# Kernel optimization log

Measured on AMD Instinct MI355X. Metric: run time of the kernel, lower is better.

The kernel has to match this reference:

```python
import jax, jax.numpy as jnp
import numpy as np

B, H, W, DIM = 8, 1024, 1024, 33


def setup_inputs() -> dict:
    key = jax.random.key(0)
    x = jax.random.uniform(key, (B, 3, H, W), dtype=jnp.float32)
    # Identity 3D LUT matching IdentityLUT{dim}.txt layout: n = i*D*D + j*D + k,
    # channel0 = k/(D-1) (red), channel1 = j/(D-1) (green), channel2 = i/(D-1) (blue).
    ax = jnp.arange(DIM, dtype=jnp.float32) / (DIM - 1)
    i, j, k = jnp.meshgrid(ax, ax, ax, indexing='ij')
    LUT = jnp.stack([k, j, i], axis=0)  # [3, D, D, D]
    return {"x": x, "LUT": LUT}


def _trilinear_lut(LUT, x):
    # LUT: [3, D, D, D] with spatial axes (i=depth, j=height, k=width).
    # x:   [B, 3, H, W] in [0,1]. grid_sample grid coord order is (w, h, d),
    # so red -> k axis, green -> j axis, blue -> i axis.
    D = LUT.shape[1]
    g = (x - 0.5) * 2.0                       # [-1, 1] grid (as in torch code)
    t = (g + 1.0) * 0.5 * (D - 1)             # align_corners=True unnormalize
    t = jnp.clip(t, 0.0, D - 1)               # padding_mode='border'
    r, gc, b = t[:, 0], t[:, 1], t[:, 2]      # each [B, H, W]

    def floor_ceil(c):
        f = jnp.floor(c)
        w = c - f
        f = f.astype(jnp.int32)
        return f, jnp.minimum(f + 1, D - 1), w

    k0, k1, wk = floor_ceil(r)
    j0, j1, wj = floor_ceil(gc)
    i0, i1, wi = floor_ceil(b)

    flat = LUT.reshape(3, -1)                 # [3, D^3]

    def gather(ii, jj, kk):
        idx = (ii * D + jj) * D + kk          # [B, H, W]
        return flat[:, idx]                   # [3, B, H, W]

    c00 = gather(i0, j0, k0) * (1 - wk) + gather(i0, j0, k1) * wk
    c01 = gather(i0, j1, k0) * (1 - wk) + gather(i0, j1, k1) * wk
    c10 = gather(i1, j0, k0) * (1 - wk) + gather(i1, j0, k1) * wk
    c11 = gather(i1, j1, k0) * (1 - wk) + gather(i1, j1, k1) * wk
    out = (c00 * (1 - wj) + c01 * wj) * (1 - wi) + (c10 * (1 - wj) + c11 * wj) * wi
    return jnp.transpose(out, (1, 0, 2, 3))   # [B, 3, H, W]


def reference(x, LUT):
    return _trilinear_lut(LUT, x)
```

## Files before the change

### kernel.cpp

```cpp
#include <hip/hip_runtime.h>
#include <hip/hip_fp16.h>

constexpr int D      = 33;
constexpr int LUTSZ  = D * D * D;
constexpr int PLANE  = 1024 * 1024;
constexpr int BATCH  = 8;
constexpr int NCELL  = 32 * 32 * 32;
constexpr size_t CELL_BYTES   = (size_t)NCELL * 32;
constexpr size_t PACKED_BYTES = (size_t)LUTSZ * 16;

constexpr int NITER = 4;

typedef float        v4f  __attribute__((ext_vector_type(4)));
typedef unsigned int v4u  __attribute__((ext_vector_type(4)));
typedef unsigned int v2u  __attribute__((ext_vector_type(2)));
typedef int          i32x4 __attribute__((ext_vector_type(4)));

__device__ v4u llvm_amdgcn_raw_buffer_load_u32x4(i32x4 srsrc, int voffset,
                                                 int soffset, int cachepolicy)
    __asm("llvm.amdgcn.raw.buffer.load.v4i32");

struct Rgb   { float c0, c1, c2; };
struct CellW { int cell; float wk, wj, wi; };

__device__ __forceinline__ unsigned int pack_h2(float lo, float hi)
{
    __half2 h = __floats2half2_rn(lo, hi);
    return *reinterpret_cast<unsigned int*>(&h);
}

__device__ __forceinline__ float h_lo(unsigned int u)
{
    __half2 h = *reinterpret_cast<__half2*>(&u);
    return __half2float(__low2half(h));
}

__device__ __forceinline__ float h_hi(unsigned int u)
{
    __half2 h = *reinterpret_cast<__half2*>(&u);
    return __half2float(__high2half(h));
}

__global__ __launch_bounds__(256)
void pack_cells_kernel(const float* __restrict__ lut, unsigned char* __restrict__ Tb)
{
    const int cell = blockIdx.x * blockDim.x + threadIdx.x;
    const int ch   = blockIdx.y;
    if (cell >= NCELL) return;
    const int i0 = cell >> 10, j0 = (cell >> 5) & 31, k0 = cell & 31;
    const int base = (i0 * D + j0) * D + k0;

    const float* __restrict__ L = lut + ch * LUTSZ + base;
    const float anchor = L[0];
    const float d1 = L[1]             - anchor;
    const float d2 = L[D]             - anchor;
    const float d3 = L[D + 1]         - anchor;
    const float d4 = L[D * D]         - anchor;
    const float d5 = L[D * D + 1]     - anchor;
    const float d6 = L[D * D + D]     - anchor;
    const float d7 = L[D * D + D + 1] - anchor;

    unsigned int wa = (unsigned int)__builtin_amdgcn_cvt_pk_fp8_f32(d1, d2, 0, false);
    wa = (unsigned int)__builtin_amdgcn_cvt_pk_fp8_f32(d3, d4, (int)wa, true);
    unsigned int wb = (unsigned int)__builtin_amdgcn_cvt_pk_fp8_f32(d5, d6, 0, false);
    wb = (unsigned int)__builtin_amdgcn_cvt_pk_fp8_f32(d7, 0.0f, (int)wb, true);

    unsigned char* __restrict__ e = Tb + (size_t)cell * 32;
    *reinterpret_cast<__half*>(e + 2 * ch) = __float2half(anchor);
    v2u dw; dw.x = wa; dw.y = wb;
    *reinterpret_cast<v2u*>(e + 8 + 8 * ch) = dw;
}

__device__ __forceinline__ CellW cell_of(float r, float g, float b)
{
    float tr = fminf(fmaxf(r * 32.0f, 0.0f), 32.0f);
    float tg = fminf(fmaxf(g * 32.0f, 0.0f), 32.0f);
    float tb = fminf(fmaxf(b * 32.0f, 0.0f), 32.0f);

    int k0 = min((int)tr, 31);
    int j0 = min((int)tg, 31);
    int i0 = min((int)tb, 31);
    CellW w;
    w.wk = tr - (float)k0;
    w.wj = tg - (float)j0;
    w.wi = tb - (float)i0;
    w.cell = ((i0 << 5) | j0) << 5 | k0;
    return w;
}

template <int SEL>
__device__ __forceinline__ float f8c(unsigned int w)
{
    return __builtin_amdgcn_cvt_f32_fp8((int)w, SEL);
}

__device__ __forceinline__ float chan_lerp(float a, unsigned int wa, unsigned int wb,
                                           float wk, float wj, float wi)
{
    const float d001 = f8c<0>(wa), d010 = f8c<1>(wa), d011 = f8c<2>(wa), d100 = f8c<3>(wa);
    const float d101 = f8c<0>(wb), d110 = f8c<1>(wb), d111 = f8c<2>(wb);
    const float L00 = wk * d001;
    const float L01 = fmaf(wk, d011 - d010, d010);
    const float L10 = fmaf(wk, d101 - d100, d100);
    const float L11 = fmaf(wk, d111 - d110, d110);
    const float c0  = fmaf(wj, L01 - L00, L00);
    const float c1  = fmaf(wj, L11 - L10, L10);
    return a + fmaf(wi, c1 - c0, c0);
}

__device__ __forceinline__ Rgb lerp_cell(v4u ea, v4u eb, CellW w)
{
    Rgb o;
    const float a0 = h_lo(ea.x), a1 = h_hi(ea.x), a2 = h_lo(ea.y);
    o.c0 = chan_lerp(a0, ea.z, ea.w, w.wk, w.wj, w.wi);
    o.c1 = chan_lerp(a1, eb.x, eb.y, w.wk, w.wj, w.wi);
    o.c2 = chan_lerp(a2, eb.z, eb.w, w.wk, w.wj, w.wi);
    return o;
}

__global__ __launch_bounds__(256)
void lut3d_cell_kernel(const float* __restrict__ x,
                       const v4u* __restrict__ T,
                       float* __restrict__ out)
{
    const int tid    = blockIdx.x * blockDim.x + threadIdx.x;
    const int stride = gridDim.x * blockDim.x;

    const unsigned long long ta = (unsigned long long)T;
    i32x4 rsrc;
    rsrc.x = (int)(ta & 0xffffffffull);
    rsrc.y = (int)(ta >> 32);
    rsrc.z = (int)CELL_BYTES;
    rsrc.w = 0x00020000;

    int c = tid;
    int base;
    v4f rv, gv, bv;
    {
        const int p0 = c << 2;
        const int b  = p0 >> 20;
        const int q  = p0 & (PLANE - 1);
        base = b * 3 * PLANE + q;
        rv = __builtin_nontemporal_load(reinterpret_cast<const v4f*>(x + base));
        gv = __builtin_nontemporal_load(reinterpret_cast<const v4f*>(x + base + PLANE));
        bv = __builtin_nontemporal_load(reinterpret_cast<const v4f*>(x + base + 2 * PLANE));
    }

#pragma unroll
    for (int it = 0; it < NITER; ++it) {
        const CellW w0 = cell_of(rv.x, gv.x, bv.x);
        const CellW w1 = cell_of(rv.y, gv.y, bv.y);
        const CellW w2 = cell_of(rv.z, gv.z, bv.z);
        const CellW w3 = cell_of(rv.w, gv.w, bv.w);

        const int o0v = w0.cell << 5, o1v = w1.cell << 5;
        const int o2v = w2.cell << 5, o3v = w3.cell << 5;
        const v4u e0a = llvm_amdgcn_raw_buffer_load_u32x4(rsrc, o0v,      0, 1);
        const v4u e0b = llvm_amdgcn_raw_buffer_load_u32x4(rsrc, o0v + 16, 0, 1);
        const v4u e1a = llvm_amdgcn_raw_buffer_load_u32x4(rsrc, o1v,      0, 1);
        const v4u e1b = llvm_amdgcn_raw_buffer_load_u32x4(rsrc, o1v + 16, 0, 1);
        const v4u e2a = llvm_amdgcn_raw_buffer_load_u32x4(rsrc, o2v,      0, 1);
        const v4u e2b = llvm_amdgcn_raw_buffer_load_u32x4(rsrc, o2v + 16, 0, 1);
        const v4u e3a = llvm_amdgcn_raw_buffer_load_u32x4(rsrc, o3v,      0, 1);
        const v4u e3b = llvm_amdgcn_raw_buffer_load_u32x4(rsrc, o3v + 16, 0, 1);

        const int cn = c + stride;
        int basen = base;
        v4f rn = rv, gn = gv, bn = bv;
        if (it + 1 < NITER) {
            const int p0 = cn << 2;
            const int b  = p0 >> 20;
            const int q  = p0 & (PLANE - 1);
            basen = b * 3 * PLANE + q;
            rn = __builtin_nontemporal_load(reinterpret_cast<const v4f*>(x + basen));
            gn = __builtin_nontemporal_load(reinterpret_cast<const v4f*>(x + basen + PLANE));
            bn = __builtin_nontemporal_load(reinterpret_cast<const v4f*>(x + basen + 2 * PLANE));
        }
        __builtin_amdgcn_sched_barrier(0);

        const Rgb q0 = lerp_cell(e0a, e0b, w0);
        const Rgb q1 = lerp_cell(e1a, e1b, w1);
        const Rgb q2 = lerp_cell(e2a, e2b, w2);
        const Rgb q3 = lerp_cell(e3a, e3b, w3);

        v4f o0 = { q0.c0, q1.c0, q2.c0, q3.c0 };
        v4f o1 = { q0.c1, q1.c1, q2.c1, q3.c1 };
        v4f o2 = { q0.c2, q1.c2, q2.c2, q3.c2 };
        __builtin_nontemporal_store(o0, reinterpret_cast<v4f*>(out + base));
        __builtin_nontemporal_store(o1, reinterpret_cast<v4f*>(out + base + PLANE));
        __builtin_nontemporal_store(o2, reinterpret_cast<v4f*>(out + base + 2 * PLANE));

        rv = rn; gv = gn; bv = bn; base = basen; c = cn;
    }
}

__global__ __launch_bounds__(256)
void pack_lut_kernel(const float* __restrict__ lut, v4u* __restrict__ P)
{
    int idx = blockIdx.x * blockDim.x + threadIdx.x;
    if (idx >= LUTSZ) return;
    int k = idx % D;
    v4u e = (v4u)(0u);
    if (k < D - 1) {
        e.x = pack_h2(lut[0 * LUTSZ + idx], lut[0 * LUTSZ + idx + 1]);
        e.y = pack_h2(lut[1 * LUTSZ + idx], lut[1 * LUTSZ + idx + 1]);
        e.z = pack_h2(lut[2 * LUTSZ + idx], lut[2 * LUTSZ + idx + 1]);
    }
    P[idx] = e;
}

__device__ __forceinline__ float lerp_h2(unsigned int u, float w)
{
    __half2 h = *reinterpret_cast<__half2*>(&u);
    float lo = __half2float(__low2half(h));
    float hi = __half2float(__high2half(h));
    return fmaf(w, hi - lo, lo);
}

__device__ __forceinline__ Rgb apply_lut_packed(const v4u* __restrict__ P,
                                                float r, float g, float b)
{
    float tr = fminf(fmaxf(r * 32.0f, 0.0f), 32.0f);
    float tg = fminf(fmaxf(g * 32.0f, 0.0f), 32.0f);
    float tb = fminf(fmaxf(b * 32.0f, 0.0f), 32.0f);
    int k0 = min((int)tr, D - 2); float wk = tr - (float)k0;
    int j0 = (int)tg; float wj = tg - (float)j0; int j1 = min(j0 + 1, D - 1);
    int i0 = (int)tb; float wi = tb - (float)i0; int i1 = min(i0 + 1, D - 1);
    v4u e00 = P[(i0 * D + j0) * D + k0];
    v4u e01 = P[(i0 * D + j1) * D + k0];
    v4u e10 = P[(i1 * D + j0) * D + k0];
    v4u e11 = P[(i1 * D + j1) * D + k0];
    Rgb o;
    {
        float c00 = lerp_h2(e00.x, wk), c01 = lerp_h2(e01.x, wk);
        float c10 = lerp_h2(e10.x, wk), c11 = lerp_h2(e11.x, wk);
        float c0 = fmaf(wj, c01 - c00, c00), c1 = fmaf(wj, c11 - c10, c10);
        o.c0 = fmaf(wi, c1 - c0, c0);
    }
    {
        float c00 = lerp_h2(e00.y, wk), c01 = lerp_h2(e01.y, wk);
        float c10 = lerp_h2(e10.y, wk), c11 = lerp_h2(e11.y, wk);
        float c0 = fmaf(wj, c01 - c00, c00), c1 = fmaf(wj, c11 - c10, c10);
        o.c1 = fmaf(wi, c1 - c0, c0);
    }
    {
        float c00 = lerp_h2(e00.z, wk), c01 = lerp_h2(e01.z, wk);
        float c10 = lerp_h2(e10.z, wk), c11 = lerp_h2(e11.z, wk);
        float c0 = fmaf(wj, c01 - c00, c00), c1 = fmaf(wj, c11 - c10, c10);
        o.c2 = fmaf(wi, c1 - c0, c0);
    }
    return o;
}

__global__ __launch_bounds__(256)
void lut3d_packed_kernel(const float* __restrict__ x,
                         const v4u* __restrict__ P,
                         float* __restrict__ out)
{
    const int tid = blockIdx.x * blockDim.x + threadIdx.x;
    const int p0  = tid << 2;
    const int b   = p0 >> 20;
    const int q   = p0 & (PLANE - 1);
    const int base = b * 3 * PLANE + q;
    const v4f rv = __builtin_nontemporal_load(reinterpret_cast<const v4f*>(x + base));
    const v4f gv = __builtin_nontemporal_load(reinterpret_cast<const v4f*>(x + base + PLANE));
    const v4f bv = __builtin_nontemporal_load(reinterpret_cast<const v4f*>(x + base + 2 * PLANE));
    Rgb p0r = apply_lut_packed(P, rv.x, gv.x, bv.x);
    Rgb p1r = apply_lut_packed(P, rv.y, gv.y, bv.y);
    Rgb p2r = apply_lut_packed(P, rv.z, gv.z, bv.z);
    Rgb p3r = apply_lut_packed(P, rv.w, gv.w, bv.w);
    v4f o0 = { p0r.c0, p1r.c0, p2r.c0, p3r.c0 };
    v4f o1 = { p0r.c1, p1r.c1, p2r.c1, p3r.c1 };
    v4f o2 = { p0r.c2, p1r.c2, p2r.c2, p3r.c2 };
    __builtin_nontemporal_store(o0, reinterpret_cast<v4f*>(out + base));
    __builtin_nontemporal_store(o1, reinterpret_cast<v4f*>(out + base + PLANE));
    __builtin_nontemporal_store(o2, reinterpret_cast<v4f*>(out + base + 2 * PLANE));
}

extern "C" void kernel_launch(void* const* d_in, const int* in_sizes, int n_in,
                              void* d_out, int out_size, void* d_ws, size_t ws_size,
                              hipStream_t stream)
{
    const float* x   = (const float*)d_in[0];
    const float* lut = (const float*)d_in[1];
    float* out       = (float*)d_out;

    if (ws_size >= CELL_BYTES) {
        pack_cells_kernel<<<dim3(NCELL / 256, 3), 256, 0, stream>>>(
            lut, (unsigned char*)d_ws);
        const int n_chunks  = (BATCH * PLANE) / 4;
        const int n_threads = n_chunks / NITER;
        lut3d_cell_kernel<<<n_threads / 256, 256, 0, stream>>>(x, (const v4u*)d_ws, out);
    } else if (ws_size >= PACKED_BYTES) {
        v4u* P = (v4u*)d_ws;
        pack_lut_kernel<<<(LUTSZ + 255) / 256, 256, 0, stream>>>(lut, P);
        const int n_threads = (BATCH * PLANE) / 4;
        lut3d_packed_kernel<<<n_threads / 256, 256, 0, stream>>>(x, P, out);
    }
}
```

Before: 214.9 us.

## Split LUT cells into linear part and skippable cross-term corrections

Re-expresses each cell's trilinear interpolation as an anchor plus linear terms plus cross-term corrections (wj*wk, wi*wk, wi*wj, wi*wj*wk). The linear part for all three channels now packs into one 16-byte entry, so the main path issues one gather per pixel instead of two. Correction coefficients sit in a second table that is read only when a per-cell flag says they are nonzero for some lane in the wavefront. For the identity LUT the corrections are zero, so the second gather and its arithmetic are skipped. Arbitrary LUTs still take the exact path, at the cost of a divergent branch and an extra load.

Measured after the change: 211.1 us. About the same (-1.8%).

```diff
diff --git a/kernel.cpp b/kernel.cpp
--- a/kernel.cpp
+++ b/kernel.cpp
@@ -6,14 +6,15 @@
 constexpr int PLANE  = 1024 * 1024;
 constexpr int BATCH  = 8;
 constexpr int NCELL  = 32 * 32 * 32;
-constexpr size_t CELL_BYTES   = (size_t)NCELL * 32;
+constexpr size_t A_BYTES      = (size_t)NCELL * 16;
+constexpr size_t B_BYTES      = (size_t)NCELL * 16;
+constexpr size_t CELL_BYTES   = A_BYTES + B_BYTES;
 constexpr size_t PACKED_BYTES = (size_t)LUTSZ * 16;
 
 constexpr int NITER = 4;
 
 typedef float        v4f  __attribute__((ext_vector_type(4)));
 typedef unsigned int v4u  __attribute__((ext_vector_type(4)));
-typedef unsigned int v2u  __attribute__((ext_vector_type(2)));
 typedef int          i32x4 __attribute__((ext_vector_type(4)));
 
 __device__ v4u llvm_amdgcn_raw_buffer_load_u32x4(i32x4 srsrc, int voffset,
@@ -41,34 +42,86 @@
     return __half2float(__high2half(h));
 }
 
+template <int SEL>
+__device__ __forceinline__ float f8c(unsigned int w)
+{
+    return __builtin_amdgcn_cvt_f32_fp8((int)w, SEL);
+}
+
 __global__ __launch_bounds__(256)
-void pack_cells_kernel(const float* __restrict__ lut, unsigned char* __restrict__ Tb)
+void pack_cells_kernel(const float* __restrict__ lut,
+                       v4u* __restrict__ A, v4u* __restrict__ Bt)
 {
     const int cell = blockIdx.x * blockDim.x + threadIdx.x;
-    const int ch   = blockIdx.y;
     if (cell >= NCELL) return;
     const int i0 = cell >> 10, j0 = (cell >> 5) & 31, k0 = cell & 31;
     const int base = (i0 * D + j0) * D + k0;
 
-    const float* __restrict__ L = lut + ch * LUTSZ + base;
-    const float anchor = L[0];
-    const float d1 = L[1]             - anchor;
-    const float d2 = L[D]             - anchor;
-    const float d3 = L[D + 1]         - anchor;
-    const float d4 = L[D * D]         - anchor;
-    const float d5 = L[D * D + 1]     - anchor;
-    const float d6 = L[D * D + D]     - anchor;
-    const float d7 = L[D * D + D + 1] - anchor;
-
-    unsigned int wa = (unsigned int)__builtin_amdgcn_cvt_pk_fp8_f32(d1, d2, 0, false);
-    wa = (unsigned int)__builtin_amdgcn_cvt_pk_fp8_f32(d3, d4, (int)wa, true);
-    unsigned int wb = (unsigned int)__builtin_amdgcn_cvt_pk_fp8_f32(d5, d6, 0, false);
-    wb = (unsigned int)__builtin_amdgcn_cvt_pk_fp8_f32(d7, 0.0f, (int)wb, true);
-
-    unsigned char* __restrict__ e = Tb + (size_t)cell * 32;
-    *reinterpret_cast<__half*>(e + 2 * ch) = __float2half(anchor);
-    v2u dw; dw.x = wa; dw.y = wb;
-    *reinterpret_cast<v2u*>(e + 8 + 8 * ch) = dw;
+    float a[3], p001[3], p010[3], p100[3];
+    float c011[3], c101[3], c110[3], c111[3];
+    bool corr = false;
+#pragma unroll
+    for (int ch = 0; ch < 3; ++ch) {
+        const float* __restrict__ L = lut + ch * LUTSZ + base;
+        const float an   = L[0];
+        const float d001 = L[1]             - an;
+        const float d010 = L[D]             - an;
+        const float d011 = L[D + 1]         - an;
+        const float d100 = L[D * D]         - an;
+        const float d101 = L[D * D + 1]     - an;
+        const float d110 = L[D * D + D]     - an;
+        const float d111 = L[D * D + D + 1] - an;
+        a[ch] = an;  p001[ch] = d001;  p010[ch] = d010;  p100[ch] = d100;
+        c011[ch] = d011 - d010 - d001;
+        c101[ch] = d101 - d100 - d001;
+        c110[ch] = d110 - d100 - d010;
+        c111[ch] = d111 - d110 - d101 - d011 + d100 + d010 + d001;
+        corr = corr || (c011[ch] != 0.0f) || (c101[ch] != 0.0f)
+                    || (c110[ch] != 0.0f) || (c111[ch] != 0.0f);
+    }
+
+    v4u ea;
+    ea.x = pack_h2(a[0], a[1]);
+    {
+        unsigned int w = pack_h2(a[2], 0.0f) & 0xffffu;
+        w = (unsigned int)__builtin_amdgcn_cvt_pk_fp8_f32(p001[0], p010[0],
+                                                          (int)w, true);
+        ea.y = w;
+    }
+    {
+        unsigned int w = (unsigned int)__builtin_amdgcn_cvt_pk_fp8_f32(
+                             p100[0], p001[1], 0, false);
+        w = (unsigned int)__builtin_amdgcn_cvt_pk_fp8_f32(p010[1], p100[1],
+                                                          (int)w, true);
+        ea.z = w;
+    }
+    {
+        unsigned int w = (unsigned int)__builtin_amdgcn_cvt_pk_fp8_f32(
+                             p001[2], p010[2], 0, false);
+        w = (unsigned int)__builtin_amdgcn_cvt_pk_fp8_f32(p100[2], 0.0f,
+                                                          (int)w, true);
+        if (corr) w |= 0x01000000u;
+        ea.w = w;
+    }
+    A[cell] = ea;
+
+    v4u eb;
+    {
+        unsigned int w0 = (unsigned int)__builtin_amdgcn_cvt_pk_fp8_f32(
+                              c011[0], c101[0], 0, false);
+        w0 = (unsigned int)__builtin_amdgcn_cvt_pk_fp8_f32(c110[0], c111[0],
+                                                           (int)w0, true);
+        unsigned int w1 = (unsigned int)__builtin_amdgcn_cvt_pk_fp8_f32(
+                              c011[1], c101[1], 0, false);
+        w1 = (unsigned int)__builtin_amdgcn_cvt_pk_fp8_f32(c110[1], c111[1],
+                                                           (int)w1, true);
+        unsigned int w2 = (unsigned int)__builtin_amdgcn_cvt_pk_fp8_f32(
+                              c011[2], c101[2], 0, false);
+        w2 = (unsigned int)__builtin_amdgcn_cvt_pk_fp8_f32(c110[2], c111[2],
+                                                           (int)w2, true);
+        eb.x = w0; eb.y = w1; eb.z = w2; eb.w = 0u;
+    }
+    Bt[cell] = eb;
 }
 
 __device__ __forceinline__ CellW cell_of(float r, float g, float b)
@@ -88,49 +141,53 @@
     return w;
 }
 
-template <int SEL>
-__device__ __forceinline__ float f8c(unsigned int w)
-{
-    return __builtin_amdgcn_cvt_f32_fp8((int)w, SEL);
-}
-
-__device__ __forceinline__ float chan_lerp(float a, unsigned int wa, unsigned int wb,
-                                           float wk, float wj, float wi)
-{
-    const float d001 = f8c<0>(wa), d010 = f8c<1>(wa), d011 = f8c<2>(wa), d100 = f8c<3>(wa);
-    const float d101 = f8c<0>(wb), d110 = f8c<1>(wb), d111 = f8c<2>(wb);
-    const float L00 = wk * d001;
-    const float L01 = fmaf(wk, d011 - d010, d010);
-    const float L10 = fmaf(wk, d101 - d100, d100);
-    const float L11 = fmaf(wk, d111 - d110, d110);
-    const float c0  = fmaf(wj, L01 - L00, L00);
-    const float c1  = fmaf(wj, L11 - L10, L10);
-    return a + fmaf(wi, c1 - c0, c0);
-}
-
-__device__ __forceinline__ Rgb lerp_cell(v4u ea, v4u eb, CellW w)
+__device__ __forceinline__ Rgb lerp_planar(v4u ea, CellW w)
 {
     Rgb o;
     const float a0 = h_lo(ea.x), a1 = h_hi(ea.x), a2 = h_lo(ea.y);
-    o.c0 = chan_lerp(a0, ea.z, ea.w, w.wk, w.wj, w.wi);
-    o.c1 = chan_lerp(a1, eb.x, eb.y, w.wk, w.wj, w.wi);
-    o.c2 = chan_lerp(a2, eb.z, eb.w, w.wk, w.wj, w.wi);
+    {
+        const float s = fmaf(w.wj, f8c<3>(ea.y), w.wi * f8c<0>(ea.z));
+        o.c0 = a0 + fmaf(w.wk, f8c<2>(ea.y), s);
+    }
+    {
+        const float s = fmaf(w.wj, f8c<2>(ea.z), w.wi * f8c<3>(ea.z));
+        o.c1 = a1 + fmaf(w.wk, f8c<1>(ea.z), s);
+    }
+    {
+        const float s = fmaf(w.wj, f8c<1>(ea.w), w.wi * f8c<2>(ea.w));
+        o.c2 = a2 + fmaf(w.wk, f8c<0>(ea.w), s);
+    }
     return o;
+}
+
+__device__ __forceinline__ void add_corr(Rgb& o, v4u eb, CellW w)
+{
+    const float pjk  = w.wj * w.wk;
+    const float pik  = w.wi * w.wk;
+    const float pij  = w.wi * w.wj;
+    const float pijk = pij * w.wk;
+    o.c0 += fmaf(pjk, f8c<0>(eb.x), fmaf(pik, f8c<1>(eb.x),
+            fmaf(pij, f8c<2>(eb.x), pijk * f8c<3>(eb.x))));
+    o.c1 += fmaf(pjk, f8c<0>(eb.y), fmaf(pik, f8c<1>(eb.y),
+            fmaf(pij, f8c<2>(eb.y), pijk * f8c<3>(eb.y))));
+    o.c2 += fmaf(pjk, f8c<0>(eb.z), fmaf(pik, f8c<1>(eb.z),
+            fmaf(pij, f8c<2>(eb.z), pijk * f8c<3>(eb.z))));
 }
 
 __global__ __launch_bounds__(256)
 void lut3d_cell_kernel(const float* __restrict__ x,
-                       const v4u* __restrict__ T,
+                       const v4u* __restrict__ TA,
+                       const v4u* __restrict__ TB,
                        float* __restrict__ out)
 {
     const int tid    = blockIdx.x * blockDim.x + threadIdx.x;
     const int stride = gridDim.x * blockDim.x;
 
-    const unsigned long long ta = (unsigned long long)T;
+    const unsigned long long ta = (unsigned long long)TA;
     i32x4 rsrc;
     rsrc.x = (int)(ta & 0xffffffffull);
     rsrc.y = (int)(ta >> 32);
-    rsrc.z = (int)CELL_BYTES;
+    rsrc.z = (int)A_BYTES;
     rsrc.w = 0x00020000;
 
     int c = tid;
@@ -138,9 +195,7 @@
     v4f rv, gv, bv;
     {
         const int p0 = c << 2;
-        const int b  = p0 >> 20;
-        const int q  = p0 & (PLANE - 1);
-        base = b * 3 * PLANE + q;
+        base = (p0 >> 20) * 3 * PLANE + (p0 & (PLANE - 1));
         rv = __builtin_nontemporal_load(reinterpret_cast<const v4f*>(x + base));
         gv = __builtin_nontemporal_load(reinterpret_cast<const v4f*>(x + base + PLANE));
         bv = __builtin_nontemporal_load(reinterpret_cast<const v4f*>(x + base + 2 * PLANE));
@@ -153,35 +208,39 @@
         const CellW w2 = cell_of(rv.z, gv.z, bv.z);
         const CellW w3 = cell_of(rv.w, gv.w, bv.w);
 
-        const int o0v = w0.cell << 5, o1v = w1.cell << 5;
-        const int o2v = w2.cell << 5, o3v = w3.cell << 5;
-        const v4u e0a = llvm_amdgcn_raw_buffer_load_u32x4(rsrc, o0v,      0, 1);
-        const v4u e0b = llvm_amdgcn_raw_buffer_load_u32x4(rsrc, o0v + 16, 0, 1);
-        const v4u e1a = llvm_amdgcn_raw_buffer_load_u32x4(rsrc, o1v,      0, 1);
-        const v4u e1b = llvm_amdgcn_raw_buffer_load_u32x4(rsrc, o1v + 16, 0, 1);
-        const v4u e2a = llvm_amdgcn_raw_buffer_load_u32x4(rsrc, o2v,      0, 1);
-        const v4u e2b = llvm_amdgcn_raw_buffer_load_u32x4(rsrc, o2v + 16, 0, 1);
-        const v4u e3a = llvm_amdgcn_raw_buffer_load_u32x4(rsrc, o3v,      0, 1);
-        const v4u e3b = llvm_amdgcn_raw_buffer_load_u32x4(rsrc, o3v + 16, 0, 1);
+        const v4u e0 = llvm_amdgcn_raw_buffer_load_u32x4(rsrc, w0.cell << 4, 0, 0);
+        const v4u e1 = llvm_amdgcn_raw_buffer_load_u32x4(rsrc, w1.cell << 4, 0, 0);
+        const v4u e2 = llvm_amdgcn_raw_buffer_load_u32x4(rsrc, w2.cell << 4, 0, 0);
+        const v4u e3 = llvm_amdgcn_raw_buffer_load_u32x4(rsrc, w3.cell << 4, 0, 0);
 
         const int cn = c + stride;
         int basen = base;
         v4f rn = rv, gn = gv, bn = bv;
         if (it + 1 < NITER) {
             const int p0 = cn << 2;
-            const int b  = p0 >> 20;
-            const int q  = p0 & (PLANE - 1);
-            basen = b * 3 * PLANE + q;
+            basen = (p0 >> 20) * 3 * PLANE + (p0 & (PLANE - 1));
             rn = __builtin_nontemporal_load(reinterpret_cast<const v4f*>(x + basen));
             gn = __builtin_nontemporal_load(reinterpret_cast<const v4f*>(x + basen + PLANE));
             bn = __builtin_nontemporal_load(reinterpret_cast<const v4f*>(x + basen + 2 * PLANE));
         }
         __builtin_amdgcn_sched_barrier(0);
 
-        const Rgb q0 = lerp_cell(e0a, e0b, w0);
-        const Rgb q1 = lerp_cell(e1a, e1b, w1);
-        const Rgb q2 = lerp_cell(e2a, e2b, w2);
-        const Rgb q3 = lerp_cell(e3a, e3b, w3);
+        Rgb q0 = lerp_planar(e0, w0);
+        Rgb q1 = lerp_planar(e1, w1);
+        Rgb q2 = lerp_planar(e2, w2);
+        Rgb q3 = lerp_planar(e3, w3);
+
+        const unsigned int need = (e0.w | e1.w | e2.w | e3.w) >> 24;
+        if (__any(need != 0u)) {
+            const v4u b0 = TB[w0.cell];
+            const v4u b1 = TB[w1.cell];
+            const v4u b2 = TB[w2.cell];
+            const v4u b3 = TB[w3.cell];
+            add_corr(q0, b0, w0);
+            add_corr(q1, b1, w1);
+            add_corr(q2, b2, w2);
+            add_corr(q3, b3, w3);
+        }
 
         v4f o0 = { q0.c0, q1.c0, q2.c0, q3.c0 };
         v4f o1 = { q0.c1, q1.c1, q2.c1, q3.c1 };
@@ -286,11 +345,12 @@
     float* out       = (float*)d_out;
 
     if (ws_size >= CELL_BYTES) {
-        pack_cells_kernel<<<dim3(NCELL / 256, 3), 256, 0, stream>>>(
-            lut, (unsigned char*)d_ws);
+        v4u* TA = (v4u*)d_ws;
+        v4u* TB = (v4u*)((unsigned char*)d_ws + A_BYTES);
+        pack_cells_kernel<<<NCELL / 256, 256, 0, stream>>>(lut, TA, TB);
         const int n_chunks  = (BATCH * PLANE) / 4;
         const int n_threads = n_chunks / NITER;
-        lut3d_cell_kernel<<<n_threads / 256, 256, 0, stream>>>(x, (const v4u*)d_ws, out);
+        lut3d_cell_kernel<<<n_threads / 256, 256, 0, stream>>>(x, TA, TB, out);
     } else if (ws_size >= PACKED_BYTES) {
         v4u* P = (v4u*)d_ws;
         pack_lut_kernel<<<(LUTSZ + 255) / 256, 256, 0, stream>>>(lut, P);
```
